# Optimization experiments

Hardware: AMD Instinct MI355X
Metric: run time of the kernel (lower is better)

## Reference

```python
import jax, jax.numpy as jnp
import numpy as np

TOP_K = 100
MIN_CONF = 0.1


def setup_inputs() -> dict:
    key = jax.random.key(0)
    points_heatmap = jax.random.uniform(key, (16, 84, 256, 256), dtype=jnp.float32)
    return {"points_heatmap": points_heatmap}


def reference(points_heatmap) -> jnp.ndarray:
    b, c_tot, h, w = points_heatmap.shape
    c = c_tot - 4  # number of class channels; last 4 are y-off, x-off, height, width

    # top-k over flattened class heatmap [b, c*h*w]
    flat = points_heatmap[:, :c].reshape(b, c * h * w)
    confidence, indices = jax.lax.top_k(flat, TOP_K)  # [b, k]

    classes = indices // (h * w)
    ind_y = (indices // w) % h
    ind_x = indices % w

    bidx = jnp.arange(b)[:, None]  # [b, 1] broadcasts against [b, k] indices
    y = ind_y.astype(jnp.float32) + points_heatmap[bidx, c, ind_y, ind_x]
    x = ind_x.astype(jnp.float32) + points_heatmap[bidx, c + 1, ind_y, ind_x]
    height = points_heatmap[bidx, c + 2, ind_y, ind_x]
    width = points_heatmap[bidx, c + 3, ind_y, ind_x]

    objects = jnp.stack(
        [y, x, height, width, classes.astype(jnp.float32), confidence], axis=-1
    )  # [b, k, 6]
    # zero entire rows whose confidence is below threshold
    objects = jnp.where(confidence[..., None] < MIN_CONF, 0.0, objects)
    return objects
```

## Files before the change

### kernel.cpp

```cpp
#include <hip/hip_runtime.h>
#include <stdint.h>

#define BATCH   16
#define C_CLS   80
#define CH_TOT  84
#define HDIM    256
#define WDIM    256
#define HW      65536
#define NCLS    (C_CLS * HW)
#define NQ      (NCLS / 4)
#define TOPK    100
#define MIN_CONF 0.1f

#define T0F     0.999f
#define T1_MONO 0xBF7D70A4u

#define LCAP    256

typedef unsigned long long u64;

__device__ __forceinline__ uint32_t mono32(uint32_t u) {
    return u ^ ((uint32_t)((int32_t)u >> 31) | 0x80000000u);
}
__device__ __forceinline__ u64 umax64(u64 a, u64 b) { return a > b ? a : b; }

__global__ __launch_bounds__(256)
void k_scan(const float* __restrict__ in, uint32_t* __restrict__ cnt0,
            uint32_t* __restrict__ ovf, u64* __restrict__ cand0,
            int cap, int bpb) {
    const int b = blockIdx.y;
    const float4* __restrict__ src =
        (const float4*)(in + (size_t)b * CH_TOT * HW);

    __shared__ uint32_t lcnt;
    __shared__ uint32_t sbase;
    __shared__ u64 lkeys[LCAP];
    if (threadIdx.x == 0) lcnt = 0;
    __syncthreads();

    const int qblk = NQ / bpb;
    const int q0 = blockIdx.x * qblk + threadIdx.x;
    const int iters = qblk / 256;

#define PROC(v, q)                                                          \
    {                                                                       \
        const float mx = fmaxf(fmaxf(v.x, v.y), fmaxf(v.z, v.w));           \
        if (mx >= T0F) {                                                    \
            const uint32_t i0 = (uint32_t)(q) * 4u;                         \
            const float e0 = v.x, e1 = v.y, e2 = v.z, e3 = v.w;             \
            if (e0 >= T0F) {                                                \
                uint32_t s = atomicAdd(&lcnt, 1u);                          \
                if (s < LCAP) lkeys[s] = ((u64)mono32(__float_as_uint(e0)) << 32) | (u64)(0xFFFFFFFFu - (i0 + 0)); \
            }                                                               \
            if (e1 >= T0F) {                                                \
                uint32_t s = atomicAdd(&lcnt, 1u);                          \
                if (s < LCAP) lkeys[s] = ((u64)mono32(__float_as_uint(e1)) << 32) | (u64)(0xFFFFFFFFu - (i0 + 1)); \
            }                                                               \
            if (e2 >= T0F) {                                                \
                uint32_t s = atomicAdd(&lcnt, 1u);                          \
                if (s < LCAP) lkeys[s] = ((u64)mono32(__float_as_uint(e2)) << 32) | (u64)(0xFFFFFFFFu - (i0 + 2)); \
            }                                                               \
            if (e3 >= T0F) {                                                \
                uint32_t s = atomicAdd(&lcnt, 1u);                          \
                if (s < LCAP) lkeys[s] = ((u64)mono32(__float_as_uint(e3)) << 32) | (u64)(0xFFFFFFFFu - (i0 + 3)); \
            }                                                               \
        }                                                                   \
    }

    for (int i = 0; i < iters; i += 4) {
        const int qa = q0 + (i + 0) * 256;
        const int qb = q0 + (i + 1) * 256;
        const int qc = q0 + (i + 2) * 256;
        const int qd = q0 + (i + 3) * 256;
        float4 va = src[qa];
        float4 vb = src[qb];
        float4 vc = src[qc];
        float4 vd = src[qd];
        PROC(va, qa)
        PROC(vb, qb)
        PROC(vc, qc)
        PROC(vd, qd)
    }
#undef PROC

    __syncthreads();
    if (threadIdx.x == 0) {
        const uint32_t n = lcnt;
        const uint32_t nn = n < LCAP ? n : LCAP;
        const uint32_t base = atomicAdd(&cnt0[b * 16], nn);
        sbase = base;
        if (n > LCAP || base + nn > (uint32_t)cap) atomicOr(&ovf[b * 16], 1u);
    }
    __syncthreads();
    const uint32_t nn = lcnt < LCAP ? lcnt : LCAP;
    for (uint32_t i = threadIdx.x; i < nn; i += 256) {
        const uint32_t s = sbase + i;
        if (s < (uint32_t)cap) cand0[(size_t)b * cap + s] = lkeys[i];
    }
}

__global__ __launch_bounds__(256)
void k_hist_fb(const float* __restrict__ in, const uint32_t* __restrict__ cnt0,
               const uint32_t* __restrict__ ovf, uint32_t* __restrict__ hist,
               int cap, int hbins, int hshift, int bpb) {
    const int b = blockIdx.y;
    const uint32_t c0 = cnt0[b * 16];
    if (ovf[b * 16] == 0u && c0 >= TOPK && c0 <= (uint32_t)cap) return;

    uint32_t* __restrict__ histb = hist + (size_t)b * hbins;
    const float4* __restrict__ src =
        (const float4*)(in + (size_t)b * CH_TOT * HW);
    const int qblk = NQ / bpb;
    const int q0 = blockIdx.x * qblk + threadIdx.x;
    const int iters = qblk / 256;
    for (int i = 0; i < iters; ++i) {
        const int q = q0 + i * 256;
        float4 v = src[q];
        uint32_t us[4] = { __float_as_uint(v.x), __float_as_uint(v.y),
                           __float_as_uint(v.z), __float_as_uint(v.w) };
#pragma unroll
        for (int j = 0; j < 4; ++j) {
            uint32_t m = mono32(us[j]);
            if (m >= T1_MONO) {
                uint32_t bin = (m - T1_MONO) >> hshift;
                if (bin >= (uint32_t)hbins) bin = hbins - 1;
                atomicAdd(&histb[bin], 1u);
            }
        }
    }
}

__global__ __launch_bounds__(256)
void k_meta(const uint32_t* __restrict__ hist, const uint32_t* __restrict__ cnt0,
            const uint32_t* __restrict__ ovf, uint4* __restrict__ meta,
            int cap, int hbins, int hshift) {
    const int b = blockIdx.x;
    const uint32_t c0 = cnt0[b * 16];
    if (ovf[b * 16] == 0u && c0 >= TOPK && c0 <= (uint32_t)cap) {
        if (threadIdx.x == 0) meta[b] = make_uint4(0u, c0, 0u, 0u);
        return;
    }
    __shared__ uint32_t psum[256];
    const uint32_t* hb = hist + (size_t)b * hbins;
    const int per = hbins / 256;
    uint32_t s = 0;
    for (int i = 0; i < per; ++i) s += hb[threadIdx.x * per + i];
    psum[threadIdx.x] = s;
    __syncthreads();
    if (threadIdx.x == 0) {
        uint32_t cum = 0, thresh = 0;
        int done = 0;
        for (int t = 255; t >= 0 && !done; --t) {
            if (cum + psum[t] >= TOPK) {
                for (int i = per - 1; i >= 0; --i) {
                    const int bin = t * per + i;
                    cum += hb[bin];
                    if (cum >= TOPK) {
                        thresh = T1_MONO + ((uint32_t)bin << hshift);
                        done = 1;
                        break;
                    }
                }
            } else {
                cum += psum[t];
            }
        }
        if (!done) thresh = 0u;
        meta[b] = make_uint4(1u, 0u, thresh, 0u);
    }
}

__global__ __launch_bounds__(256)
void k_collect2(const float* __restrict__ in, const uint4* __restrict__ meta,
                uint32_t* __restrict__ cnt1, u64* __restrict__ cand1,
                int cap, int bpb) {
    const int b = blockIdx.y;
    const uint4 m = meta[b];
    if (m.x != 1u) return;
    const uint32_t thresh = m.z;
    const float4* __restrict__ src =
        (const float4*)(in + (size_t)b * CH_TOT * HW);
    const int qblk = NQ / bpb;
    const int q0 = blockIdx.x * qblk + threadIdx.x;
    const int iters = qblk / 256;
    for (int i = 0; i < iters; ++i) {
        const int q = q0 + i * 256;
        float4 v = src[q];
        uint32_t us[4] = { __float_as_uint(v.x), __float_as_uint(v.y),
                           __float_as_uint(v.z), __float_as_uint(v.w) };
        const uint32_t idx0 = (uint32_t)q * 4u;
#pragma unroll
        for (int j = 0; j < 4; ++j) {
            uint32_t mo = mono32(us[j]);
            if (mo >= thresh) {
                uint32_t slot = atomicAdd(&cnt1[b * 16], 1u);
                if (slot < (uint32_t)cap) {
                    u64 key = ((u64)mo << 32) | (u64)(0xFFFFFFFFu - (idx0 + j));
                    cand1[(size_t)b * cap + slot] = key;
                }
            }
        }
    }
}

template <int CAP>
__global__ __launch_bounds__(512)
void k_final(const float* __restrict__ in, const uint4* __restrict__ meta,
             const uint32_t* __restrict__ cnt1, const u64* __restrict__ cand0,
             const u64* __restrict__ cand1, float* __restrict__ out) {
    constexpr int NT = 512;
    constexpr int KPT = CAP / NT;
    const int b = blockIdx.x;
    const int t = threadIdx.x;
    const int wave = t >> 6, lane = t & 63;

    const uint4 m = meta[b];
    const u64* cand;
    uint32_t n;
    if (m.x == 0u) { cand = cand0 + (size_t)b * CAP; n = m.y; }
    else           { cand = cand1 + (size_t)b * CAP; n = min(cnt1[b * 16], (uint32_t)CAP); }

    u64 key[KPT];
#pragma unroll
    for (int j = 0; j < KPT; ++j) {
        const uint32_t i = (uint32_t)(t + j * NT);
        key[j] = (i < n) ? cand[i] : 0ull;
    }
    u64 lmax = 0;
#pragma unroll
    for (int j = 0; j < KPT; ++j) lmax = umax64(lmax, key[j]);

    __shared__ u64 wmax[NT / 64];
    __shared__ u64 gsel;
    __shared__ u64 sel[TOPK];

    for (int r = 0; r < TOPK; ++r) {
        u64 wm = lmax;
#pragma unroll
        for (int d = 1; d < 64; d <<= 1) wm = umax64(wm, __shfl_xor(wm, d, 64));
        if (lane == 0) wmax[wave] = wm;
        __syncthreads();
        if (t == 0) {
            u64 g = wmax[0];
#pragma unroll
            for (int w2 = 1; w2 < NT / 64; ++w2) g = umax64(g, wmax[w2]);
            gsel = g;
            sel[r] = g;
        }
        __syncthreads();
        const u64 g = gsel;
        if (g != 0ull && lmax == g) {
#pragma unroll
            for (int j = 0; j < KPT; ++j) if (key[j] == g) key[j] = 0ull;
            lmax = 0;
#pragma unroll
            for (int j = 0; j < KPT; ++j) lmax = umax64(lmax, key[j]);
        }
    }
    __syncthreads();

    if (t < TOPK) {
        const u64 kk = sel[t];
        float* o = out + ((size_t)b * TOPK + t) * 6;
        float vals[6] = {0.f, 0.f, 0.f, 0.f, 0.f, 0.f};
        if (kk != 0ull) {
            const uint32_t mo = (uint32_t)(kk >> 32);
            const uint32_t bits = (mo & 0x80000000u) ? (mo & 0x7FFFFFFFu) : ~mo;
            const float conf = __uint_as_float(bits);
            if (conf >= MIN_CONF) {
                const uint32_t idx = 0xFFFFFFFFu - (uint32_t)(kk & 0xFFFFFFFFu);
                const uint32_t cls = idx >> 16;
                const uint32_t yy = (idx >> 8) & 255u;
                const uint32_t xx = idx & 255u;
                const float* base = in + (size_t)b * CH_TOT * HW + yy * WDIM + xx;
                const float offy = base[(size_t)(C_CLS + 0) * HW];
                const float offx = base[(size_t)(C_CLS + 1) * HW];
                const float hh   = base[(size_t)(C_CLS + 2) * HW];
                const float ww   = base[(size_t)(C_CLS + 3) * HW];
                vals[0] = (float)yy + offy;
                vals[1] = (float)xx + offx;
                vals[2] = hh;
                vals[3] = ww;
                vals[4] = (float)cls;
                vals[5] = conf;
            }
        }
#pragma unroll
        for (int j = 0; j < 6; ++j) o[j] = vals[j];
    }
}

extern "C" void kernel_launch(void* const* d_in, const int* in_sizes, int n_in,
                              void* d_out, int out_size, void* d_ws, size_t ws_size,
                              hipStream_t stream) {
    const float* in = (const float*)d_in[0];
    float* out = (float*)d_out;
    uint8_t* ws = (uint8_t*)d_ws;

    const int bpb = 320;

    const size_t cntB = (size_t)BATCH * 64;
    const size_t metaB = (size_t)BATCH * 16;

    const size_t need_big = (size_t)BATCH * 4096 * 4 + 3 * cntB + metaB
                          + 2ull * BATCH * 8192 * 8;

    if (ws_size >= need_big) {
        const int CAP = 8192, HBINS = 4096, HSHIFT = 6;
        const size_t histB = (size_t)BATCH * HBINS * 4;
        uint32_t* hist = (uint32_t*)ws;
        uint32_t* cnt0 = (uint32_t*)(ws + histB);
        uint32_t* cnt1 = (uint32_t*)(ws + histB + cntB);
        uint32_t* ovf  = (uint32_t*)(ws + histB + 2 * cntB);
        uint4*    meta = (uint4*)(ws + histB + 3 * cntB);
        u64* cand0 = (u64*)(ws + histB + 3 * cntB + metaB);
        u64* cand1 = (u64*)(ws + histB + 3 * cntB + metaB + (size_t)BATCH * CAP * 8);

        hipMemsetAsync(d_ws, 0, histB + 3 * cntB, stream);
        dim3 gs(bpb, BATCH), blk(256);
        k_scan<<<gs, blk, 0, stream>>>(in, cnt0, ovf, cand0, CAP, bpb);
        k_hist_fb<<<gs, blk, 0, stream>>>(in, cnt0, ovf, hist, CAP, HBINS, HSHIFT, bpb);
        k_meta<<<BATCH, 256, 0, stream>>>(hist, cnt0, ovf, meta, CAP, HBINS, HSHIFT);
        k_collect2<<<gs, blk, 0, stream>>>(in, meta, cnt1, cand1, CAP, bpb);
        k_final<8192><<<BATCH, 512, 0, stream>>>(in, meta, cnt1, cand0, cand1, out);
    } else {
        const int CAP = 1024, HBINS = 1024, HSHIFT = 8;
        const size_t histB = (size_t)BATCH * HBINS * 4;
        uint32_t* hist = (uint32_t*)ws;
        uint32_t* cnt0 = (uint32_t*)(ws + histB);
        uint32_t* cnt1 = (uint32_t*)(ws + histB + cntB);
        uint32_t* ovf  = (uint32_t*)(ws + histB + 2 * cntB);
        uint4*    meta = (uint4*)(ws + histB + 3 * cntB);
        u64* cand0 = (u64*)(ws + histB + 3 * cntB + metaB);
        u64* cand1 = (u64*)(ws + histB + 3 * cntB + metaB + (size_t)BATCH * CAP * 8);

        hipMemsetAsync(d_ws, 0, histB + 3 * cntB, stream);
        dim3 gs(bpb, BATCH), blk(256);
        k_scan<<<gs, blk, 0, stream>>>(in, cnt0, ovf, cand0, CAP, bpb);
        k_hist_fb<<<gs, blk, 0, stream>>>(in, cnt0, ovf, hist, CAP, HBINS, HSHIFT, bpb);
        k_meta<<<BATCH, 256, 0, stream>>>(hist, cnt0, ovf, meta, CAP, HBINS, HSHIFT);
        k_collect2<<<gs, blk, 0, stream>>>(in, meta, cnt1, cand1, CAP, bpb);
        k_final<1024><<<BATCH, 512, 0, stream>>>(in, meta, cnt1, cand0, cand1, out);
    }
}
```

Measured before the change: 537.4 us.

## Replace serial top-k argmax loop with histogram-based selection and drop fallback kernel

The final kernel's 100 sequential block-wide argmax rounds are replaced by a shared-memory histogram over candidate keys that finds a cutoff bin, then a small rank-by-counting sort over the few surviving keys. The old serial loop is kept only as a fallback when too many keys survive. The separate fallback histogram pass is folded into the per-batch meta kernel using a shared-memory histogram. The workspace memset becomes a tiny init kernel, the scan loop is unrolled 8-wide and blocks per batch are halved. The intent is to cut the latency-bound serial reduction and a launch, at the cost of a slow single-block-per-batch fallback path.

```diff
diff --git a/kernel.cpp b/kernel.cpp
--- a/kernel.cpp
+++ b/kernel.cpp
@@ -1,5 +1,6 @@
 #include <hip/hip_runtime.h>
 #include <stdint.h>
+#include <string.h>
 
 #define BATCH   16
 #define C_CLS   80
@@ -12,10 +13,10 @@
 #define TOPK    100
 #define MIN_CONF 0.1f
 
-#define T0F     0.999f
 #define T1_MONO 0xBF7D70A4u
 
 #define LCAP    256
+#define BPB     160
 
 typedef unsigned long long u64;
 
@@ -23,11 +24,20 @@
     return u ^ ((uint32_t)((int32_t)u >> 31) | 0x80000000u);
 }
 __device__ __forceinline__ u64 umax64(u64 a, u64 b) { return a > b ? a : b; }
+
+__global__ __launch_bounds__(256)
+void k_init(uint32_t* __restrict__ cnt0, uint32_t* __restrict__ cnt1,
+            uint32_t* __restrict__ ovf) {
+    const int t = threadIdx.x;
+    cnt0[t] = 0u;
+    cnt1[t] = 0u;
+    ovf[t]  = 0u;
+}
 
 __global__ __launch_bounds__(256)
 void k_scan(const float* __restrict__ in, uint32_t* __restrict__ cnt0,
             uint32_t* __restrict__ ovf, u64* __restrict__ cand0,
-            int cap, int bpb) {
+            int cap, float t0f) {
     const int b = blockIdx.y;
     const float4* __restrict__ src =
         (const float4*)(in + (size_t)b * CH_TOT * HW);
@@ -38,50 +48,37 @@
     if (threadIdx.x == 0) lcnt = 0;
     __syncthreads();
 
-    const int qblk = NQ / bpb;
+    const int qblk = NQ / BPB;
     const int q0 = blockIdx.x * qblk + threadIdx.x;
     const int iters = qblk / 256;
 
-#define PROC(v, q)                                                          \
-    {                                                                       \
-        const float mx = fmaxf(fmaxf(v.x, v.y), fmaxf(v.z, v.w));           \
-        if (mx >= T0F) {                                                    \
-            const uint32_t i0 = (uint32_t)(q) * 4u;                         \
-            const float e0 = v.x, e1 = v.y, e2 = v.z, e3 = v.w;             \
-            if (e0 >= T0F) {                                                \
-                uint32_t s = atomicAdd(&lcnt, 1u);                          \
-                if (s < LCAP) lkeys[s] = ((u64)mono32(__float_as_uint(e0)) << 32) | (u64)(0xFFFFFFFFu - (i0 + 0)); \
-            }                                                               \
-            if (e1 >= T0F) {                                                \
-                uint32_t s = atomicAdd(&lcnt, 1u);                          \
-                if (s < LCAP) lkeys[s] = ((u64)mono32(__float_as_uint(e1)) << 32) | (u64)(0xFFFFFFFFu - (i0 + 1)); \
-            }                                                               \
-            if (e2 >= T0F) {                                                \
-                uint32_t s = atomicAdd(&lcnt, 1u);                          \
-                if (s < LCAP) lkeys[s] = ((u64)mono32(__float_as_uint(e2)) << 32) | (u64)(0xFFFFFFFFu - (i0 + 2)); \
-            }                                                               \
-            if (e3 >= T0F) {                                                \
-                uint32_t s = atomicAdd(&lcnt, 1u);                          \
-                if (s < LCAP) lkeys[s] = ((u64)mono32(__float_as_uint(e3)) << 32) | (u64)(0xFFFFFFFFu - (i0 + 3)); \
-            }                                                               \
-        }                                                                   \
-    }
-
-    for (int i = 0; i < iters; i += 4) {
-        const int qa = q0 + (i + 0) * 256;
-        const int qb = q0 + (i + 1) * 256;
-        const int qc = q0 + (i + 2) * 256;
-        const int qd = q0 + (i + 3) * 256;
-        float4 va = src[qa];
-        float4 vb = src[qb];
-        float4 vc = src[qc];
-        float4 vd = src[qd];
-        PROC(va, qa)
-        PROC(vb, qb)
-        PROC(vc, qc)
-        PROC(vd, qd)
-    }
-#undef PROC
+    for (int i = 0; i < iters; i += 8) {
+        float4 v[8];
+        int q[8];
+#pragma unroll
+        for (int u = 0; u < 8; ++u) {
+            q[u] = q0 + (i + u) * 256;
+            v[u] = src[q[u]];
+        }
+#pragma unroll
+        for (int u = 0; u < 8; ++u) {
+            const float4 vv = v[u];
+            const float mx = fmaxf(fmaxf(vv.x, vv.y), fmaxf(vv.z, vv.w));
+            if (mx >= t0f) {
+                const uint32_t i0 = (uint32_t)q[u] * 4u;
+                const float e[4] = { vv.x, vv.y, vv.z, vv.w };
+#pragma unroll
+                for (int j = 0; j < 4; ++j) {
+                    if (e[j] >= t0f) {
+                        uint32_t s = atomicAdd(&lcnt, 1u);
+                        if (s < LCAP)
+                            lkeys[s] = ((u64)mono32(__float_as_uint(e[j])) << 32)
+                                     | (u64)(0xFFFFFFFFu - (i0 + j));
+                    }
+                }
+            }
+        }
+    }
 
     __syncthreads();
     if (threadIdx.x == 0) {
@@ -100,69 +97,44 @@
 }
 
 __global__ __launch_bounds__(256)
-void k_hist_fb(const float* __restrict__ in, const uint32_t* __restrict__ cnt0,
-               const uint32_t* __restrict__ ovf, uint32_t* __restrict__ hist,
-               int cap, int hbins, int hshift, int bpb) {
-    const int b = blockIdx.y;
-    const uint32_t c0 = cnt0[b * 16];
-    if (ovf[b * 16] == 0u && c0 >= TOPK && c0 <= (uint32_t)cap) return;
-
-    uint32_t* __restrict__ histb = hist + (size_t)b * hbins;
-    const float4* __restrict__ src =
-        (const float4*)(in + (size_t)b * CH_TOT * HW);
-    const int qblk = NQ / bpb;
-    const int q0 = blockIdx.x * qblk + threadIdx.x;
-    const int iters = qblk / 256;
-    for (int i = 0; i < iters; ++i) {
-        const int q = q0 + i * 256;
-        float4 v = src[q];
-        uint32_t us[4] = { __float_as_uint(v.x), __float_as_uint(v.y),
-                           __float_as_uint(v.z), __float_as_uint(v.w) };
-#pragma unroll
-        for (int j = 0; j < 4; ++j) {
-            uint32_t m = mono32(us[j]);
-            if (m >= T1_MONO) {
-                uint32_t bin = (m - T1_MONO) >> hshift;
-                if (bin >= (uint32_t)hbins) bin = hbins - 1;
-                atomicAdd(&histb[bin], 1u);
-            }
-        }
-    }
-}
-
-__global__ __launch_bounds__(256)
-void k_meta(const uint32_t* __restrict__ hist, const uint32_t* __restrict__ cnt0,
+void k_meta(const float* __restrict__ in, const uint32_t* __restrict__ cnt0,
             const uint32_t* __restrict__ ovf, uint4* __restrict__ meta,
-            int cap, int hbins, int hshift) {
+            int cap) {
     const int b = blockIdx.x;
     const uint32_t c0 = cnt0[b * 16];
     if (ovf[b * 16] == 0u && c0 >= TOPK && c0 <= (uint32_t)cap) {
         if (threadIdx.x == 0) meta[b] = make_uint4(0u, c0, 0u, 0u);
         return;
     }
-    __shared__ uint32_t psum[256];
-    const uint32_t* hb = hist + (size_t)b * hbins;
-    const int per = hbins / 256;
-    uint32_t s = 0;
-    for (int i = 0; i < per; ++i) s += hb[threadIdx.x * per + i];
-    psum[threadIdx.x] = s;
+    __shared__ uint32_t hist[4096];
+    for (int i = threadIdx.x; i < 4096; i += 256) hist[i] = 0u;
+    __syncthreads();
+    const float4* __restrict__ src =
+        (const float4*)(in + (size_t)b * CH_TOT * HW);
+    for (int q = threadIdx.x; q < NQ; q += 256) {
+        float4 v = src[q];
+        uint32_t us[4] = { __float_as_uint(v.x), __float_as_uint(v.y),
+                           __float_as_uint(v.z), __float_as_uint(v.w) };
+#pragma unroll
+        for (int j = 0; j < 4; ++j) {
+            uint32_t m = mono32(us[j]);
+            if (m >= T1_MONO) {
+                uint32_t bin = (m - T1_MONO) >> 6;
+                if (bin > 4095u) bin = 4095u;
+                atomicAdd(&hist[bin], 1u);
+            }
+        }
+    }
     __syncthreads();
     if (threadIdx.x == 0) {
         uint32_t cum = 0, thresh = 0;
         int done = 0;
-        for (int t = 255; t >= 0 && !done; --t) {
-            if (cum + psum[t] >= TOPK) {
-                for (int i = per - 1; i >= 0; --i) {
-                    const int bin = t * per + i;
-                    cum += hb[bin];
-                    if (cum >= TOPK) {
-                        thresh = T1_MONO + ((uint32_t)bin << hshift);
-                        done = 1;
-                        break;
-                    }
-                }
-            } else {
-                cum += psum[t];
+        for (int t = 4095; t >= 0; --t) {
+            cum += hist[t];
+            if (cum >= TOPK) {
+                thresh = T1_MONO + ((uint32_t)t << 6);
+                done = 1;
+                break;
             }
         }
         if (!done) thresh = 0u;
@@ -173,14 +145,14 @@
 __global__ __launch_bounds__(256)
 void k_collect2(const float* __restrict__ in, const uint4* __restrict__ meta,
                 uint32_t* __restrict__ cnt1, u64* __restrict__ cand1,
-                int cap, int bpb) {
+                int cap) {
     const int b = blockIdx.y;
     const uint4 m = meta[b];
     if (m.x != 1u) return;
     const uint32_t thresh = m.z;
     const float4* __restrict__ src =
         (const float4*)(in + (size_t)b * CH_TOT * HW);
-    const int qblk = NQ / bpb;
+    const int qblk = NQ / BPB;
     const int q0 = blockIdx.x * qblk + threadIdx.x;
     const int iters = qblk / 256;
     for (int i = 0; i < iters; ++i) {
@@ -207,9 +179,11 @@
 __global__ __launch_bounds__(512)
 void k_final(const float* __restrict__ in, const uint4* __restrict__ meta,
              const uint32_t* __restrict__ cnt1, const u64* __restrict__ cand0,
-             const u64* __restrict__ cand1, float* __restrict__ out) {
+             const u64* __restrict__ cand1, float* __restrict__ out,
+             uint32_t binbase, int binshift) {
     constexpr int NT = 512;
     constexpr int KPT = CAP / NT;
+    constexpr int SELCAP = 512;
     const int b = blockIdx.x;
     const int t = threadIdx.x;
     const int wave = t >> 6, lane = t & 63;
@@ -219,6 +193,7 @@
     uint32_t n;
     if (m.x == 0u) { cand = cand0 + (size_t)b * CAP; n = m.y; }
     else           { cand = cand1 + (size_t)b * CAP; n = min(cnt1[b * 16], (uint32_t)CAP); }
+    if (n > (uint32_t)CAP) n = (uint32_t)CAP;
 
     u64 key[KPT];
 #pragma unroll
@@ -226,38 +201,108 @@
         const uint32_t i = (uint32_t)(t + j * NT);
         key[j] = (i < n) ? cand[i] : 0ull;
     }
-    u64 lmax = 0;
-#pragma unroll
-    for (int j = 0; j < KPT; ++j) lmax = umax64(lmax, key[j]);
-
-    __shared__ u64 wmax[NT / 64];
-    __shared__ u64 gsel;
+
+    __shared__ uint32_t hist[4096];
+    __shared__ uint32_t psum[NT];
+    __shared__ u64 skeys[SELCAP];
+    __shared__ uint32_t scnt;
     __shared__ u64 sel[TOPK];
-
-    for (int r = 0; r < TOPK; ++r) {
-        u64 wm = lmax;
-#pragma unroll
-        for (int d = 1; d < 64; d <<= 1) wm = umax64(wm, __shfl_xor(wm, d, 64));
-        if (lane == 0) wmax[wave] = wm;
+    __shared__ uint32_t sB, sS;
+
+    for (int i = t; i < 4096; i += NT) hist[i] = 0u;
+    if (t < TOPK) sel[t] = 0ull;
+    if (t == 0) scnt = 0u;
+    __syncthreads();
+
+#define KBIN(kk)                                                            \
+    ({ const uint32_t mo_ = (uint32_t)((kk) >> 32);                         \
+       uint32_t bin_ = 0u;                                                  \
+       if (mo_ >= binbase) {                                                \
+           bin_ = (mo_ - binbase) >> binshift;                              \
+           if (bin_ > 4095u) bin_ = 4095u;                                  \
+       }                                                                    \
+       bin_; })
+
+#pragma unroll
+    for (int j = 0; j < KPT; ++j)
+        if (key[j] != 0ull) atomicAdd(&hist[KBIN(key[j])], 1u);
+    __syncthreads();
+
+    uint32_t ps = 0;
+#pragma unroll
+    for (int i = 0; i < 8; ++i) ps += hist[t * 8 + i];
+    psum[t] = ps;
+    __syncthreads();
+    if (t == 0) {
+        uint32_t cum = 0;
+        uint32_t B = 0, S = 0;
+        int done = 0;
+        for (int seg = NT - 1; seg >= 0 && !done; --seg) {
+            if (cum + psum[seg] >= TOPK) {
+                for (int i = 7; i >= 0; --i) {
+                    const int bin = seg * 8 + i;
+                    cum += hist[bin];
+                    if (cum >= TOPK) { B = (uint32_t)bin; S = cum; done = 1; break; }
+                }
+            } else {
+                cum += psum[seg];
+            }
+        }
+        if (!done) { B = 0u; S = cum; }
+        sB = B; sS = S;
+    }
+    __syncthreads();
+    const uint32_t B = sB, S = sS;
+
+    if (S <= (uint32_t)SELCAP) {
+#pragma unroll
+        for (int j = 0; j < KPT; ++j) {
+            if (key[j] != 0ull && KBIN(key[j]) >= B) {
+                uint32_t s = atomicAdd(&scnt, 1u);
+                if (s < (uint32_t)SELCAP) skeys[s] = key[j];
+            }
+        }
         __syncthreads();
-        if (t == 0) {
-            u64 g = wmax[0];
-#pragma unroll
-            for (int w2 = 1; w2 < NT / 64; ++w2) g = umax64(g, wmax[w2]);
-            gsel = g;
-            sel[r] = g;
+        const uint32_t Sc = scnt < (uint32_t)SELCAP ? scnt : (uint32_t)SELCAP;
+        for (uint32_t i = t; i < Sc; i += NT) {
+            const u64 kk = skeys[i];
+            uint32_t r = 0;
+            for (uint32_t j2 = 0; j2 < Sc; ++j2) r += (skeys[j2] > kk) ? 1u : 0u;
+            if (r < TOPK) sel[r] = kk;
         }
         __syncthreads();
-        const u64 g = gsel;
-        if (g != 0ull && lmax == g) {
-#pragma unroll
-            for (int j = 0; j < KPT; ++j) if (key[j] == g) key[j] = 0ull;
-            lmax = 0;
-#pragma unroll
-            for (int j = 0; j < KPT; ++j) lmax = umax64(lmax, key[j]);
-        }
-    }
-    __syncthreads();
+    } else {
+        u64 lmax = 0;
+#pragma unroll
+        for (int j = 0; j < KPT; ++j) lmax = umax64(lmax, key[j]);
+        __shared__ u64 wmax[NT / 64];
+        __shared__ u64 gsel;
+        for (int r = 0; r < TOPK; ++r) {
+            u64 wm = lmax;
+#pragma unroll
+            for (int d = 1; d < 64; d <<= 1) wm = umax64(wm, __shfl_xor(wm, d, 64));
+            if (lane == 0) wmax[wave] = wm;
+            __syncthreads();
+            if (t == 0) {
+                u64 g = wmax[0];
+#pragma unroll
+                for (int w2 = 1; w2 < NT / 64; ++w2) g = umax64(g, wmax[w2]);
+                gsel = g;
+                sel[r] = g;
+            }
+            __syncthreads();
+            const u64 g = gsel;
+            if (g != 0ull && lmax == g) {
+#pragma unroll
+                for (int j = 0; j < KPT; ++j) if (key[j] == g) key[j] = 0ull;
+                lmax = 0;
+#pragma unroll
+                for (int j = 0; j < KPT; ++j) lmax = umax64(lmax, key[j]);
+            }
+        }
+        __syncthreads();
+    }
+#undef KBIN
 
     if (t < TOPK) {
         const u64 kk = sel[t];
@@ -297,49 +342,50 @@
     float* out = (float*)d_out;
     uint8_t* ws = (uint8_t*)d_ws;
 
-    const int bpb = 320;
-
     const size_t cntB = (size_t)BATCH * 64;
     const size_t metaB = (size_t)BATCH * 16;
 
-    const size_t need_big = (size_t)BATCH * 4096 * 4 + 3 * cntB + metaB
-                          + 2ull * BATCH * 8192 * 8;
+    auto monoh = [](float f) -> uint32_t {
+        uint32_t u;
+        memcpy(&u, &f, 4);
+        return u ^ ((uint32_t)((int32_t)u >> 31) | 0x80000000u);
+    };
+
+    const size_t need_big = 3 * cntB + metaB + 2ull * BATCH * 8192 * 8;
+
+    dim3 gs(BPB, BATCH), blk(256);
 
     if (ws_size >= need_big) {
-        const int CAP = 8192, HBINS = 4096, HSHIFT = 6;
-        const size_t histB = (size_t)BATCH * HBINS * 4;
-        uint32_t* hist = (uint32_t*)ws;
-        uint32_t* cnt0 = (uint32_t*)(ws + histB);
-        uint32_t* cnt1 = (uint32_t*)(ws + histB + cntB);
-        uint32_t* ovf  = (uint32_t*)(ws + histB + 2 * cntB);
-        uint4*    meta = (uint4*)(ws + histB + 3 * cntB);
-        u64* cand0 = (u64*)(ws + histB + 3 * cntB + metaB);
-        u64* cand1 = (u64*)(ws + histB + 3 * cntB + metaB + (size_t)BATCH * CAP * 8);
-
-        hipMemsetAsync(d_ws, 0, histB + 3 * cntB, stream);
-        dim3 gs(bpb, BATCH), blk(256);
-        k_scan<<<gs, blk, 0, stream>>>(in, cnt0, ovf, cand0, CAP, bpb);
-        k_hist_fb<<<gs, blk, 0, stream>>>(in, cnt0, ovf, hist, CAP, HBINS, HSHIFT, bpb);
-        k_meta<<<BATCH, 256, 0, stream>>>(hist, cnt0, ovf, meta, CAP, HBINS, HSHIFT);
-        k_collect2<<<gs, blk, 0, stream>>>(in, meta, cnt1, cand1, CAP, bpb);
-        k_final<8192><<<BATCH, 512, 0, stream>>>(in, meta, cnt1, cand0, cand1, out);
+        const int CAP = 8192;
+        const float T0 = 0.999f;
+        uint32_t* cnt0 = (uint32_t*)ws;
+        uint32_t* cnt1 = (uint32_t*)(ws + cntB);
+        uint32_t* ovf  = (uint32_t*)(ws + 2 * cntB);
+        uint4*    meta = (uint4*)(ws + 3 * cntB);
+        u64* cand0 = (u64*)(ws + 3 * cntB + metaB);
+        u64* cand1 = (u64*)(ws + 3 * cntB + metaB + (size_t)BATCH * CAP * 8);
+
+        k_init<<<1, 256, 0, stream>>>(cnt0, cnt1, ovf);
+        k_scan<<<gs, blk, 0, stream>>>(in, cnt0, ovf, cand0, CAP, T0);
+        k_meta<<<BATCH, 256, 0, stream>>>(in, cnt0, ovf, meta, CAP);
+        k_collect2<<<gs, blk, 0, stream>>>(in, meta, cnt1, cand1, CAP);
+        k_final<8192><<<BATCH, 512, 0, stream>>>(in, meta, cnt1, cand0, cand1,
+                                                 out, monoh(T0), 3);
     } else {
-        const int CAP = 1024, HBINS = 1024, HSHIFT = 8;
-        const size_t histB = (size_t)BATCH * HBINS * 4;
-        uint32_t* hist = (uint32_t*)ws;
-        uint32_t* cnt0 = (uint32_t*)(ws + histB);
-        uint32_t* cnt1 = (uint32_t*)(ws + histB + cntB);
-        uint32_t* ovf  = (uint32_t*)(ws + histB + 2 * cntB);
-        uint4*    meta = (uint4*)(ws + histB + 3 * cntB);
-        u64* cand0 = (u64*)(ws + histB + 3 * cntB + metaB);
-        u64* cand1 = (u64*)(ws + histB + 3 * cntB + metaB + (size_t)BATCH * CAP * 8);
-
-        hipMemsetAsync(d_ws, 0, histB + 3 * cntB, stream);
-        dim3 gs(bpb, BATCH), blk(256);
-        k_scan<<<gs, blk, 0, stream>>>(in, cnt0, ovf, cand0, CAP, bpb);
-        k_hist_fb<<<gs, blk, 0, stream>>>(in, cnt0, ovf, hist, CAP, HBINS, HSHIFT, bpb);
-        k_meta<<<BATCH, 256, 0, stream>>>(hist, cnt0, ovf, meta, CAP, HBINS, HSHIFT);
-        k_collect2<<<gs, blk, 0, stream>>>(in, meta, cnt1, cand1, CAP, bpb);
-        k_final<1024><<<BATCH, 512, 0, stream>>>(in, meta, cnt1, cand0, cand1, out);
-    }
-}
+        const int CAP = 1024;
+        const float T0 = 0.99995f;
+        uint32_t* cnt0 = (uint32_t*)ws;
+        uint32_t* cnt1 = (uint32_t*)(ws + cntB);
+        uint32_t* ovf  = (uint32_t*)(ws + 2 * cntB);
+        uint4*    meta = (uint4*)(ws + 3 * cntB);
+        u64* cand0 = (u64*)(ws + 3 * cntB + metaB);
+        u64* cand1 = (u64*)(ws + 3 * cntB + metaB + (size_t)BATCH * CAP * 8);
+
+        k_init<<<1, 256, 0, stream>>>(cnt0, cnt1, ovf);
+        k_scan<<<gs, blk, 0, stream>>>(in, cnt0, ovf, cand0, CAP, T0);
+        k_meta<<<BATCH, 256, 0, stream>>>(in, cnt0, ovf, meta, CAP);
+        k_collect2<<<gs, blk, 0, stream>>>(in, meta, cnt1, cand1, CAP);
+        k_final<1024><<<BATCH, 512, 0, stream>>>(in, meta, cnt1, cand0, cand1,
+                                                 out, monoh(T0), 0);
+    }
+}
```

Result: faster. 483.7 us (-10.0%).
